# Kernel tuning notes

Hardware: AMD Instinct MI355X
Metric: run time of the kernel (lower is better)

The kernel has to match this reference:

```python
import jax, jax.numpy as jnp
import numpy as np

B, T, S, H = 8, 512, 512, 128


def setup_inputs() -> dict:
    key = jax.random.key(0)
    ks = jax.random.split(key, 8)
    query = jax.random.normal(ks[0], (B, T, H), dtype=jnp.float32)
    encoder_outputs = jax.random.normal(ks[1], (B, S, H), dtype=jnp.float32)
    src_lengths = jax.random.randint(ks[2], (B,), 1, S + 1)
    src_lengths = src_lengths.at[0].set(S)  # torch mask width == lengths.max() must equal S
    scale = 1.0 / np.sqrt(H)
    W_h = jax.random.normal(ks[3], (H, H), dtype=jnp.float32) * scale
    W_s = jax.random.normal(ks[4], (H, H), dtype=jnp.float32) * scale
    v = jax.random.normal(ks[5], (H,), dtype=jnp.float32) * scale
    W_out_w = jax.random.normal(ks[6], (H, 2 * H), dtype=jnp.float32) * (1.0 / np.sqrt(2 * H))
    W_out_b = jax.random.normal(ks[7], (H,), dtype=jnp.float32) * 0.01
    return {"query": query, "encoder_outputs": encoder_outputs,
            "src_lengths": src_lengths, "W_h": W_h, "W_s": W_s, "v": v,
            "W_out_w": W_out_w, "W_out_b": W_out_b}


def reference(query, encoder_outputs, src_lengths, W_h, W_s, v, W_out_w, W_out_b):
    # query: (B,T,H); encoder_outputs: (B,S,H)
    S_ = encoder_outputs.shape[1]
    WS = jnp.einsum('bth,oh->bto', query, W_s)            # (B,T,H)
    WH = jnp.einsum('bsh,oh->bso', encoder_outputs, W_h)  # (B,S,H)
    # additive scores: v^T tanh(W_s s_t + W_h h_i)  -> (B,T,S)
    scores = jnp.einsum('btsh,h->bts', jnp.tanh(WS[:, :, None, :] + WH[:, None, :, :]), v)
    mask = jnp.arange(S_) < src_lengths[:, None]          # (B,S)
    # faithful quirk: original zeroes (not -inf) masked scores before softmax
    scores = jnp.where(mask[:, None, :], scores, 0.0)
    attn = jax.nn.softmax(scores, axis=-1)                # (B,T,S)
    ct = jnp.einsum('bts,bsh->bth', attn, encoder_outputs)
    concat = jnp.concatenate([ct, query], axis=-1)        # (B,T,2H)
    return jnp.tanh(jnp.einsum('btc,oc->bto', concat, W_out_w) + W_out_b)
```

## Files before the change

kernel.cpp:

```cpp
#include <hip/hip_runtime.h>

#define NB 8
#define NT 512
#define NS 512
#define NH 128
#define C2LOG2E 2.8853900817779268f

__device__ __forceinline__ float fast_exp2(float x) { return __builtin_amdgcn_exp2f(x); }
__device__ __forceinline__ float fast_rcp(float x)  { return __builtin_amdgcn_rcpf(x); }
__device__ __forceinline__ float fast_tanh(float x) {
  float e = fast_exp2(x * C2LOG2E);
  return 1.0f - 2.0f * fast_rcp(e + 1.0f);
}

__device__ __forceinline__ float dot4(float4 a, float4 b) {
  return (a.x * b.x + a.y * b.y) + (a.z * b.z + a.w * b.w);
}

__device__ __forceinline__ float2 pair_acc2(float e0, float e1, float v0, float v1,
                                            float2 f0, float2 f1, float2 acc) {
  float2 P0, P1, num, den;
  P0.x = fmaf(e0, f0.x, 1.0f); P0.y = fmaf(e0, f0.y, 1.0f);
  P1.x = fmaf(e1, f1.x, 1.0f); P1.y = fmaf(e1, f1.y, 1.0f);
  num.x = fmaf(v0, P1.x, v1 * P0.x); num.y = fmaf(v0, P1.y, v1 * P0.y);
  den.x = P0.x * P1.x; den.y = P0.y * P1.y;
  acc.x = fmaf(num.x, fast_rcp(den.x), acc.x);
  acc.y = fmaf(num.y, fast_rcp(den.y), acc.y);
  return acc;
}

__device__ __forceinline__ float4 pair_acc(float e0, float e1, float v0, float v1,
                                           float4 f0, float4 f1, float4 acc) {
  float4 P0, P1, num, den;
  P0.x = fmaf(e0, f0.x, 1.0f); P0.y = fmaf(e0, f0.y, 1.0f);
  P0.z = fmaf(e0, f0.z, 1.0f); P0.w = fmaf(e0, f0.w, 1.0f);
  P1.x = fmaf(e1, f1.x, 1.0f); P1.y = fmaf(e1, f1.y, 1.0f);
  P1.z = fmaf(e1, f1.z, 1.0f); P1.w = fmaf(e1, f1.w, 1.0f);
  num.x = fmaf(v0, P1.x, v1 * P0.x); num.y = fmaf(v0, P1.y, v1 * P0.y);
  num.z = fmaf(v0, P1.z, v1 * P0.z); num.w = fmaf(v0, P1.w, v1 * P0.w);
  den.x = P0.x * P1.x; den.y = P0.y * P1.y;
  den.z = P0.z * P1.z; den.w = P0.w * P1.w;
  acc.x = fmaf(num.x, fast_rcp(den.x), acc.x);
  acc.y = fmaf(num.y, fast_rcp(den.y), acc.y);
  acc.z = fmaf(num.z, fast_rcp(den.z), acc.z);
  acc.w = fmaf(num.w, fast_rcp(den.w), acc.w);
  return acc;
}

__global__ __launch_bounds__(256) void bah_proj_kernel(
    const float* __restrict__ query, const float* __restrict__ enc,
    const float* __restrict__ W_s, const float* __restrict__ W_h,
    float* __restrict__ EWS, float* __restrict__ EWHT) {
  __shared__ __align__(16) float lds_w[64 * 132];
  __shared__ __align__(16) float lds_x[32 * 132];
  int blk = blockIdx.x;
  const bool is_wh = blk >= 256;
  const float* in = is_wh ? enc : query;
  const float* W  = is_wh ? W_h : W_s;
  blk &= 255;
  const int rb = blk >> 1, ch = blk & 1;
  const int r0 = rb * 32, c0 = ch * 64;
  const int tid = threadIdx.x;
  for (int i = tid; i < 2048; i += 256) {
    int r = i >> 5, c4 = i & 31;
    *(float4*)(lds_w + r * 132 + c4 * 4) =
        *(const float4*)(W + (c0 + r) * 128 + c4 * 4);
  }
  for (int i = tid; i < 1024; i += 256) {
    int r = i >> 5, c4 = i & 31;
    *(float4*)(lds_x + r * 132 + c4 * 4) =
        *(const float4*)(in + (r0 + r) * NH + c4 * 4);
  }
  __syncthreads();
  const int cg = tid & 31;
  const int rg = tid >> 5;
  float acc[4][2] = {{0,0},{0,0},{0,0},{0,0}};
  for (int k4 = 0; k4 < 32; ++k4) {
    float4 xa[4], wb[2];
    #pragma unroll
    for (int i = 0; i < 4; ++i)
      xa[i] = *(const float4*)(lds_x + (rg * 4 + i) * 132 + k4 * 4);
    #pragma unroll
    for (int m = 0; m < 2; ++m)
      wb[m] = *(const float4*)(lds_w + (cg + 32 * m) * 132 + k4 * 4);
    #pragma unroll
    for (int i = 0; i < 4; ++i)
      #pragma unroll
      for (int m = 0; m < 2; ++m)
        acc[i][m] += dot4(xa[i], wb[m]);
  }
  if (!is_wh) {
    #pragma unroll
    for (int i = 0; i < 4; ++i)
      #pragma unroll
      for (int m = 0; m < 2; ++m)
        EWS[(r0 + rg * 4 + i) * NH + c0 + cg + 32 * m] =
            fast_exp2(C2LOG2E * acc[i][m]);
  } else {
    __syncthreads();
    #pragma unroll
    for (int i = 0; i < 4; ++i)
      #pragma unroll
      for (int m = 0; m < 2; ++m)
        lds_x[(cg + 32 * m) * 33 + rg * 4 + i] = fast_exp2(C2LOG2E * acc[i][m]);
    __syncthreads();
    const int b = r0 >> 9, sl0 = r0 & 511;
    const int s_lane = tid & 31, hr = tid >> 5;
    #pragma unroll
    for (int j = 0; j < 8; ++j)
      EWHT[b * NH * NS + (c0 + hr * 8 + j) * NS + sl0 + s_lane] =
          lds_x[(hr * 8 + j) * 33 + s_lane];
  }
}

__global__ __launch_bounds__(256) void bah_score_kernel(
    const float* __restrict__ EWS, const float* __restrict__ EWHT,
    const float* __restrict__ v, const int* __restrict__ src_len,
    float* __restrict__ SC) {
  __shared__ __align__(16) float lds_et[8 * 132];
  __shared__ __align__(16) float lds_v[128];
  const int blk = blockIdx.x;
  const int sh = blk & 1, tt8 = (blk >> 1) & 63, bb = blk >> 7;
  const int s0 = sh * 256, t0 = tt8 * 8;
  const int len = src_len[bb];
  const int tid = threadIdx.x;
  const int tg = tid >> 7, sp = tid & 127;
  const int sbase = s0 + sp * 2;
  float* scb = SC + (bb * NT + t0) * NS;
  if (len <= s0) {
    float2 z = {0.f, 0.f};
    #pragma unroll
    for (int tt = 0; tt < 4; ++tt)
      *(float2*)(scb + (tg * 4 + tt) * NS + sbase) = z;
    return;
  }
  if (tid < 32) *(float4*)(lds_v + tid * 4) = *(const float4*)(v + tid * 4);
  { int r = tid >> 5, c4 = tid & 31;
    *(float4*)(lds_et + r * 132 + c4 * 4) =
        *(const float4*)(EWS + (bb * NT + t0 + r) * NH + c4 * 4); }
  __syncthreads();
  float V0 = 0.f;
  #pragma unroll
  for (int i = 0; i < 32; ++i) {
    float4 t4 = *(const float4*)(lds_v + i * 4);
    V0 += (t4.x + t4.y) + (t4.z + t4.w);
  }
  const float* et = lds_et + tg * 4 * 132;
  const float* fb = EWHT + bb * NH * NS + sbase;
  float2 acc2[4] = {{0,0},{0,0},{0,0},{0,0}};
  for (int ho = 0; ho < 16; ++ho) {
    const float* fh = fb + ho * 8 * NS;
    float2 F0 = *(const float2*)(fh + 0 * NS);
    float2 F1 = *(const float2*)(fh + 1 * NS);
    float2 F2 = *(const float2*)(fh + 2 * NS);
    float2 F3 = *(const float2*)(fh + 3 * NS);
    float2 F4 = *(const float2*)(fh + 4 * NS);
    float2 F5 = *(const float2*)(fh + 5 * NS);
    float2 F6 = *(const float2*)(fh + 6 * NS);
    float2 F7 = *(const float2*)(fh + 7 * NS);
    float4 va = *(const float4*)(lds_v + ho * 8);
    float4 vb = *(const float4*)(lds_v + ho * 8 + 4);
    #pragma unroll
    for (int tt = 0; tt < 4; ++tt) {
      float4 e0 = *(const float4*)(et + tt * 132 + ho * 8);
      float4 e1 = *(const float4*)(et + tt * 132 + ho * 8 + 4);
      acc2[tt] = pair_acc2(e0.x, e0.y, va.x, va.y, F0, F1, acc2[tt]);
      acc2[tt] = pair_acc2(e0.z, e0.w, va.z, va.w, F2, F3, acc2[tt]);
      acc2[tt] = pair_acc2(e1.x, e1.y, vb.x, vb.y, F4, F5, acc2[tt]);
      acc2[tt] = pair_acc2(e1.z, e1.w, vb.z, vb.w, F6, F7, acc2[tt]);
    }
  }
  #pragma unroll
  for (int tt = 0; tt < 4; ++tt) {
    float2 r;
    r.x = (sbase + 0 < len) ? fmaf(-2.f, acc2[tt].x, V0) : 0.f;
    r.y = (sbase + 1 < len) ? fmaf(-2.f, acc2[tt].y, V0) : 0.f;
    *(float2*)(scb + (tg * 4 + tt) * NS + sbase) = r;
  }
}

__global__ __launch_bounds__(256) void bah_ctx_kernel(
    const float* __restrict__ SC, const float* __restrict__ enc,
    float* __restrict__ CT) {
  __shared__ __align__(16) float lds_sc[4 * 516];
  __shared__ __align__(16) float lds_aT[512 * 4];
  __shared__ float red[16];
  const int tid = threadIdx.x;
  const int bb = blockIdx.x >> 7;
  const int t0 = (blockIdx.x & 127) * 4;
  for (int i = tid; i < 512; i += 256) {
    int r = i >> 7, c4 = i & 127;
    *(float4*)(lds_sc + r * 516 + c4 * 4) =
        *(const float4*)(SC + (bb * NT + t0 + r) * NS + c4 * 4);
  }
  __syncthreads();

  const int t = tid & 3;
  const int c = tid >> 2;
  const int wv = tid >> 6;
  float pv[8];
  float mx = -3.4e38f;
  #pragma unroll
  for (int k = 0; k < 8; ++k) {
    pv[k] = lds_sc[t * 516 + c + 64 * k];
    mx = fmaxf(mx, pv[k]);
  }
  #pragma unroll
  for (int msk = 4; msk <= 32; msk <<= 1)
    mx = fmaxf(mx, __shfl_xor(mx, msk, 64));
  if ((tid & 63) < 4) red[wv * 4 + t] = mx;
  __syncthreads();
  mx = fmaxf(fmaxf(red[t], red[4 + t]), fmaxf(red[8 + t], red[12 + t]));
  __syncthreads();
  float sum = 0.f;
  #pragma unroll
  for (int k = 0; k < 8; ++k) {
    pv[k] = fast_exp2((pv[k] - mx) * 1.4426950408889634f);
    sum += pv[k];
  }
  #pragma unroll
  for (int msk = 4; msk <= 32; msk <<= 1)
    sum += __shfl_xor(sum, msk, 64);
  if ((tid & 63) < 4) red[wv * 4 + t] = sum;
  __syncthreads();
  sum = (red[t] + red[4 + t]) + (red[8 + t] + red[12 + t]);
  const float rd = fast_rcp(sum);
  #pragma unroll
  for (int k = 0; k < 8; ++k)
    lds_aT[(c + 64 * k) * 4 + t] = pv[k] * rd;
  __syncthreads();

  const int hg = tid & 31, sg = tid >> 5;
  float4 a4[4] = {{0,0,0,0},{0,0,0,0},{0,0,0,0},{0,0,0,0}};
  const float* eb = enc + bb * NS * NH + hg * 4;
  for (int k = 0; k < 64; ++k) {
    int s = sg * 64 + k;
    float4 e = *(const float4*)(eb + s * NH);
    float4 w = *(const float4*)(lds_aT + s * 4);
    a4[0].x += w.x*e.x; a4[0].y += w.x*e.y; a4[0].z += w.x*e.z; a4[0].w += w.x*e.w;
    a4[1].x += w.y*e.x; a4[1].y += w.y*e.y; a4[1].z += w.y*e.z; a4[1].w += w.y*e.w;
    a4[2].x += w.z*e.x; a4[2].y += w.z*e.y; a4[2].z += w.z*e.z; a4[2].w += w.z*e.w;
    a4[3].x += w.w*e.x; a4[3].y += w.w*e.y; a4[3].z += w.w*e.z; a4[3].w += w.w*e.w;
  }
  #pragma unroll
  for (int i = 0; i < 4; ++i) {
    a4[i].x += __shfl_xor(a4[i].x, 32, 64);
    a4[i].y += __shfl_xor(a4[i].y, 32, 64);
    a4[i].z += __shfl_xor(a4[i].z, 32, 64);
    a4[i].w += __shfl_xor(a4[i].w, 32, 64);
  }
  float* lred = lds_sc;
  const int lane = tid & 63;
  if (lane < 32) {
    #pragma unroll
    for (int i = 0; i < 4; ++i)
      *(float4*)(lred + wv * 512 + i * 128 + hg * 4) = a4[i];
  }
  __syncthreads();
  if (tid < 128) {
    int tt = tid >> 5, hh = tid & 31;
    float4 s0 = *(const float4*)(lred + 0 * 512 + tt * 128 + hh * 4);
    float4 s1 = *(const float4*)(lred + 1 * 512 + tt * 128 + hh * 4);
    float4 s2 = *(const float4*)(lred + 2 * 512 + tt * 128 + hh * 4);
    float4 s3 = *(const float4*)(lred + 3 * 512 + tt * 128 + hh * 4);
    float4 o;
    o.x = (s0.x + s1.x) + (s2.x + s3.x);
    o.y = (s0.y + s1.y) + (s2.y + s3.y);
    o.z = (s0.z + s1.z) + (s2.z + s3.z);
    o.w = (s0.w + s1.w) + (s2.w + s3.w);
    *(float4*)(CT + (bb * NT + t0 + tt) * NH + hh * 4) = o;
  }
}

__global__ __launch_bounds__(256, 4) void bah_attn_fused(
    const float* __restrict__ EWS, const float* __restrict__ EWHT,
    const float* __restrict__ v, const float* __restrict__ enc,
    const int* __restrict__ src_len, float* __restrict__ CT) {
  __shared__ __align__(16) float lds_et[8 * 132];
  __shared__ __align__(16) float lds_v[128];
  __shared__ __align__(16) float lds_sc[8 * 516];
  __shared__ __align__(16) float lds_aT[512 * 8];
  __shared__ float red[32];
  const int tid = threadIdx.x;
  const int bb = blockIdx.x >> 6;
  const int t0 = (blockIdx.x & 63) * 8;
  const int len = src_len[bb];
  if (tid < 32) *(float4*)(lds_v + tid * 4) = *(const float4*)(v + tid * 4);
  { int r = tid >> 5, c4 = tid & 31;
    *(float4*)(lds_et + r * 132 + c4 * 4) =
        *(const float4*)(EWS + (bb * NT + t0 + r) * NH + c4 * 4); }
  __syncthreads();
  float V0 = 0.f;
  #pragma unroll
  for (int i = 0; i < 32; ++i) {
    float4 t4 = *(const float4*)(lds_v + i * 4);
    V0 += (t4.x + t4.y) + (t4.z + t4.w);
  }
  const int tg = tid >> 7, sp = tid & 127;
  const float* et = lds_et + tg * 4 * 132;
  const float* fb = EWHT + bb * NH * NS + sp * 4;
  float4 acc4[4] = {{0,0,0,0},{0,0,0,0},{0,0,0,0},{0,0,0,0}};
  for (int ho = 0; ho < 16; ++ho) {
    const float* fh = fb + ho * 8 * NS;
    float4 F0 = *(const float4*)(fh + 0 * NS);
    float4 F1 = *(const float4*)(fh + 1 * NS);
    float4 F2 = *(const float4*)(fh + 2 * NS);
    float4 F3 = *(const float4*)(fh + 3 * NS);
    float4 F4 = *(const float4*)(fh + 4 * NS);
    float4 F5 = *(const float4*)(fh + 5 * NS);
    float4 F6 = *(const float4*)(fh + 6 * NS);
    float4 F7 = *(const float4*)(fh + 7 * NS);
    float4 va = *(const float4*)(lds_v + ho * 8);
    float4 vb = *(const float4*)(lds_v + ho * 8 + 4);
    #pragma unroll
    for (int tt = 0; tt < 4; ++tt) {
      float4 e0 = *(const float4*)(et + tt * 132 + ho * 8);
      float4 e1 = *(const float4*)(et + tt * 132 + ho * 8 + 4);
      acc4[tt] = pair_acc(e0.x, e0.y, va.x, va.y, F0, F1, acc4[tt]);
      acc4[tt] = pair_acc(e0.z, e0.w, va.z, va.w, F2, F3, acc4[tt]);
      acc4[tt] = pair_acc(e1.x, e1.y, vb.x, vb.y, F4, F5, acc4[tt]);
      acc4[tt] = pair_acc(e1.z, e1.w, vb.z, vb.w, F6, F7, acc4[tt]);
    }
  }
  const int sbase = sp * 4;
  #pragma unroll
  for (int tt = 0; tt < 4; ++tt) {
    float4 r;
    r.x = (sbase + 0 < len) ? fmaf(-2.f, acc4[tt].x, V0) : 0.f;
    r.y = (sbase + 1 < len) ? fmaf(-2.f, acc4[tt].y, V0) : 0.f;
    r.z = (sbase + 2 < len) ? fmaf(-2.f, acc4[tt].z, V0) : 0.f;
    r.w = (sbase + 3 < len) ? fmaf(-2.f, acc4[tt].w, V0) : 0.f;
    *(float4*)(lds_sc + (tg * 4 + tt) * 516 + sbase) = r;
  }
  __syncthreads();
  const int t = tid & 7;
  const int c = tid >> 3;
  const int wid = tid >> 6;
  float pv[16];
  float mx = -3.4e38f;
  #pragma unroll
  for (int k = 0; k < 16; ++k) {
    pv[k] = lds_sc[t * 516 + c + 32 * k];
    mx = fmaxf(mx, pv[k]);
  }
  #pragma unroll
  for (int msk = 8; msk <= 32; msk <<= 1)
    mx = fmaxf(mx, __shfl_xor(mx, msk, 64));
  if ((tid & 63) < 8) red[wid * 8 + t] = mx;
  __syncthreads();
  mx = fmaxf(fmaxf(red[t], red[8 + t]), fmaxf(red[16 + t], red[24 + t]));
  __syncthreads();
  float sum = 0.f;
  #pragma unroll
  for (int k = 0; k < 16; ++k) {
    pv[k] = fast_exp2((pv[k] - mx) * 1.4426950408889634f);
    sum += pv[k];
  }
  #pragma unroll
  for (int msk = 8; msk <= 32; msk <<= 1)
    sum += __shfl_xor(sum, msk, 64);
  if ((tid & 63) < 8) red[wid * 8 + t] = sum;
  __syncthreads();
  sum = (red[t] + red[8 + t]) + (red[16 + t] + red[24 + t]);
  const float rd = fast_rcp(sum);
  #pragma unroll
  for (int k = 0; k < 16; ++k)
    lds_aT[(c + 32 * k) * 8 + t] = pv[k] * rd;
  __syncthreads();
  const int hg = tid & 31, sg = tid >> 5;
  float4 a8[8] = {{0,0,0,0},{0,0,0,0},{0,0,0,0},{0,0,0,0},
                  {0,0,0,0},{0,0,0,0},{0,0,0,0},{0,0,0,0}};
  const float* eb = enc + bb * NS * NH + hg * 4;
  for (int k = 0; k < 64; ++k) {
    int s = sg * 64 + k;
    float4 e  = *(const float4*)(eb + s * NH);
    float4 w0 = *(const float4*)(lds_aT + s * 8);
    float4 w1 = *(const float4*)(lds_aT + s * 8 + 4);
    a8[0].x += w0.x*e.x; a8[0].y += w0.x*e.y; a8[0].z += w0.x*e.z; a8[0].w += w0.x*e.w;
    a8[1].x += w0.y*e.x; a8[1].y += w0.y*e.y; a8[1].z += w0.y*e.z; a8[1].w += w0.y*e.w;
    a8[2].x += w0.z*e.x; a8[2].y += w0.z*e.y; a8[2].z += w0.z*e.z; a8[2].w += w0.z*e.w;
    a8[3].x += w0.w*e.x; a8[3].y += w0.w*e.y; a8[3].z += w0.w*e.z; a8[3].w += w0.w*e.w;
    a8[4].x += w1.x*e.x; a8[4].y += w1.x*e.y; a8[4].z += w1.x*e.z; a8[4].w += w1.x*e.w;
    a8[5].x += w1.y*e.x; a8[5].y += w1.y*e.y; a8[5].z += w1.y*e.z; a8[5].w += w1.y*e.w;
    a8[6].x += w1.z*e.x; a8[6].y += w1.z*e.y; a8[6].z += w1.z*e.z; a8[6].w += w1.z*e.w;
    a8[7].x += w1.w*e.x; a8[7].y += w1.w*e.y; a8[7].z += w1.w*e.z; a8[7].w += w1.w*e.w;
  }
  #pragma unroll
  for (int i = 0; i < 8; ++i) {
    a8[i].x += __shfl_xor(a8[i].x, 32, 64);
    a8[i].y += __shfl_xor(a8[i].y, 32, 64);
    a8[i].z += __shfl_xor(a8[i].z, 32, 64);
    a8[i].w += __shfl_xor(a8[i].w, 32, 64);
  }
  float* lred = lds_sc;
  const int wv = tid >> 6, lane = tid & 63;
  if (lane < 32) {
    #pragma unroll
    for (int i = 0; i < 8; ++i)
      *(float4*)(lred + wv * 1024 + i * 128 + lane * 4) = a8[i];
  }
  __syncthreads();
  { int tt2 = tid >> 5, hh = tid & 31;
    float4 s0 = *(const float4*)(lred + 0 * 1024 + tt2 * 128 + hh * 4);
    float4 s1 = *(const float4*)(lred + 1 * 1024 + tt2 * 128 + hh * 4);
    float4 s2 = *(const float4*)(lred + 2 * 1024 + tt2 * 128 + hh * 4);
    float4 s3 = *(const float4*)(lred + 3 * 1024 + tt2 * 128 + hh * 4);
    float4 o;
    o.x = (s0.x + s1.x) + (s2.x + s3.x);
    o.y = (s0.y + s1.y) + (s2.y + s3.y);
    o.z = (s0.z + s1.z) + (s2.z + s3.z);
    o.w = (s0.w + s1.w) + (s2.w + s3.w);
    *(float4*)(CT + (bb * NT + t0 + tt2) * NH + hh * 4) = o;
  }
}

__global__ __launch_bounds__(256) void bah_out_kernel(
    const float* __restrict__ CT, const float* __restrict__ query,
    const float* __restrict__ Wout, const float* __restrict__ bias,
    float* __restrict__ out) {
  __shared__ __align__(16) float lds_w[64 * 132];
  __shared__ __align__(16) float lds_x[16 * 260];
  const int rt = blockIdx.x >> 1, ch = blockIdx.x & 1;
  const int r0 = rt * 16, c0 = ch * 64;
  const int tid = threadIdx.x;
  for (int i = tid; i < 1024; i += 256) {
    int r = i >> 6, cc = (i & 63) * 4;
    float4 val = (cc < 128)
        ? *(const float4*)(CT + (r0 + r) * NH + cc)
        : *(const float4*)(query + (r0 + r) * NH + cc - 128);
    *(float4*)(lds_x + r * 260 + cc) = val;
  }
  const int cg = tid & 31;
  const int rg = tid >> 5;
  float acc[2][2] = {{0,0},{0,0}};
  for (int p = 0; p < 2; ++p) {
    __syncthreads();
    for (int i = tid; i < 2048; i += 256) {
      int r = i >> 5, c4 = i & 31;
      *(float4*)(lds_w + r * 132 + c4 * 4) =
          *(const float4*)(Wout + (c0 + r) * 256 + p * 128 + c4 * 4);
    }
    __syncthreads();
    for (int k4 = 0; k4 < 32; ++k4) {
      float4 xa[2], wb[2];
      #pragma unroll
      for (int i = 0; i < 2; ++i)
        xa[i] = *(const float4*)(lds_x + (rg * 2 + i) * 260 + p * 128 + k4 * 4);
      #pragma unroll
      for (int m = 0; m < 2; ++m)
        wb[m] = *(const float4*)(lds_w + (cg + 32 * m) * 132 + k4 * 4);
      #pragma unroll
      for (int i = 0; i < 2; ++i)
        #pragma unroll
        for (int m = 0; m < 2; ++m)
          acc[i][m] += dot4(xa[i], wb[m]);
    }
  }
  #pragma unroll
  for (int i = 0; i < 2; ++i)
    #pragma unroll
    for (int m = 0; m < 2; ++m)
      out[(r0 + rg * 2 + i) * NH + c0 + cg + 32 * m] =
          fast_tanh(acc[i][m] + bias[c0 + cg + 32 * m]);
}

extern "C" void kernel_launch(void* const* d_in, const int* in_sizes, int n_in,
                              void* d_out, int out_size, void* d_ws, size_t ws_size,
                              hipStream_t stream) {
  const float* query = (const float*)d_in[0];
  const float* enc   = (const float*)d_in[1];
  const int*   slen  = (const int*)d_in[2];
  const float* W_h   = (const float*)d_in[3];
  const float* W_s   = (const float*)d_in[4];
  const float* v     = (const float*)d_in[5];
  const float* Woutw = (const float*)d_in[6];
  const float* Woutb = (const float*)d_in[7];
  float* out = (float*)d_out;

  float* ws = (float*)d_ws;
  float* EWS  = ws;
  float* EWHT = ws + 524288;
  float* CT   = ws + 1048576;
  float* SC   = ws + 1572864;
  const bool have_sc = ws_size >= (size_t)(1572864 + 2097152) * sizeof(float);

  bah_proj_kernel<<<512, 256, 0, stream>>>(query, enc, W_s, W_h, EWS, EWHT);
  if (have_sc) {
    bah_score_kernel<<<1024, 256, 0, stream>>>(EWS, EWHT, v, slen, SC);
    bah_ctx_kernel<<<1024, 256, 0, stream>>>(SC, enc, CT);
  } else {
    bah_attn_fused<<<512, 256, 0, stream>>>(EWS, EWHT, v, enc, slen, CT);
  }
  bah_out_kernel<<<512, 256, 0, stream>>>(CT, query, Woutw, Woutb, out);
}
```

Measured before the change: 135.1 us.

## Fuse output projection into context kernel and split score work across H halves

The separate output-projection kernel is removed from the main path and its linear-plus-tanh is folded into the context kernel, reading a transposed W_out that the projection kernel now also produces in extra blocks. The score kernel now has each half of the block cover all 8 query rows over half of H, then combines the two partial sums through shared memory, instead of splitting rows. This saves one launch and a round-trip of the context tensor through global memory. In exchange it adds per-block GEMV work with global W reads in the ctx kernel, plus an extra barrier and LDS exchange in the score kernel.

```diff
diff --git a/kernel.cpp b/kernel.cpp
--- a/kernel.cpp
+++ b/kernel.cpp
@@ -50,10 +50,18 @@
 __global__ __launch_bounds__(256) void bah_proj_kernel(
     const float* __restrict__ query, const float* __restrict__ enc,
     const float* __restrict__ W_s, const float* __restrict__ W_h,
-    float* __restrict__ EWS, float* __restrict__ EWHT) {
+    const float* __restrict__ Wout,
+    float* __restrict__ EWS, float* __restrict__ EWHT, float* __restrict__ WTP) {
   __shared__ __align__(16) float lds_w[64 * 132];
   __shared__ __align__(16) float lds_x[32 * 132];
   int blk = blockIdx.x;
+  if (blk >= 512) {
+    int g = (blk - 512) * 256 + threadIdx.x;
+    int c = g >> 6, k4 = g & 63;
+    float4 w = *(const float4*)(Wout + c * 256 + k4 * 4);
+    *(float4*)(WTP + k4 * 512 + c * 4) = w;
+    return;
+  }
   const bool is_wh = blk >= 256;
   const float* in = is_wh ? enc : query;
   const float* W  = is_wh ? W_h : W_s;
@@ -119,6 +127,7 @@
     float* __restrict__ SC) {
   __shared__ __align__(16) float lds_et[8 * 132];
   __shared__ __align__(16) float lds_v[128];
+  __shared__ __align__(16) float lds_par[128 * 18];
   const int blk = blockIdx.x;
   const int sh = blk & 1, tt8 = (blk >> 1) & 63, bb = blk >> 7;
   const int s0 = sh * 256, t0 = tt8 * 8;
@@ -128,10 +137,12 @@
   const int sbase = s0 + sp * 2;
   float* scb = SC + (bb * NT + t0) * NS;
   if (len <= s0) {
-    float2 z = {0.f, 0.f};
-    #pragma unroll
-    for (int tt = 0; tt < 4; ++tt)
-      *(float2*)(scb + (tg * 4 + tt) * NS + sbase) = z;
+    if (tg == 0) {
+      float2 z = {0.f, 0.f};
+      #pragma unroll
+      for (int tt = 0; tt < 8; ++tt)
+        *(float2*)(scb + tt * NS + sbase) = z;
+    }
     return;
   }
   if (tid < 32) *(float4*)(lds_v + tid * 4) = *(const float4*)(v + tid * 4);
@@ -139,16 +150,12 @@
     *(float4*)(lds_et + r * 132 + c4 * 4) =
         *(const float4*)(EWS + (bb * NT + t0 + r) * NH + c4 * 4); }
   __syncthreads();
-  float V0 = 0.f;
-  #pragma unroll
-  for (int i = 0; i < 32; ++i) {
-    float4 t4 = *(const float4*)(lds_v + i * 4);
-    V0 += (t4.x + t4.y) + (t4.z + t4.w);
-  }
-  const float* et = lds_et + tg * 4 * 132;
-  const float* fb = EWHT + bb * NH * NS + sbase;
-  float2 acc2[4] = {{0,0},{0,0},{0,0},{0,0}};
-  for (int ho = 0; ho < 16; ++ho) {
+  const int h0 = tg * 64;
+  const float* fb = EWHT + bb * NH * NS + h0 * NS + sbase;
+  float2 acc2[8];
+  #pragma unroll
+  for (int i = 0; i < 8; ++i) { acc2[i].x = 0.f; acc2[i].y = 0.f; }
+  for (int ho = 0; ho < 8; ++ho) {
     const float* fh = fb + ho * 8 * NS;
     float2 F0 = *(const float2*)(fh + 0 * NS);
     float2 F1 = *(const float2*)(fh + 1 * NS);
@@ -158,30 +165,48 @@
     float2 F5 = *(const float2*)(fh + 5 * NS);
     float2 F6 = *(const float2*)(fh + 6 * NS);
     float2 F7 = *(const float2*)(fh + 7 * NS);
-    float4 va = *(const float4*)(lds_v + ho * 8);
-    float4 vb = *(const float4*)(lds_v + ho * 8 + 4);
-    #pragma unroll
-    for (int tt = 0; tt < 4; ++tt) {
-      float4 e0 = *(const float4*)(et + tt * 132 + ho * 8);
-      float4 e1 = *(const float4*)(et + tt * 132 + ho * 8 + 4);
+    float4 va = *(const float4*)(lds_v + h0 + ho * 8);
+    float4 vb = *(const float4*)(lds_v + h0 + ho * 8 + 4);
+    #pragma unroll
+    for (int tt = 0; tt < 8; ++tt) {
+      float4 e0 = *(const float4*)(lds_et + tt * 132 + h0 + ho * 8);
+      float4 e1 = *(const float4*)(lds_et + tt * 132 + h0 + ho * 8 + 4);
       acc2[tt] = pair_acc2(e0.x, e0.y, va.x, va.y, F0, F1, acc2[tt]);
       acc2[tt] = pair_acc2(e0.z, e0.w, va.z, va.w, F2, F3, acc2[tt]);
       acc2[tt] = pair_acc2(e1.x, e1.y, vb.x, vb.y, F4, F5, acc2[tt]);
       acc2[tt] = pair_acc2(e1.z, e1.w, vb.z, vb.w, F6, F7, acc2[tt]);
     }
   }
-  #pragma unroll
-  for (int tt = 0; tt < 4; ++tt) {
-    float2 r;
-    r.x = (sbase + 0 < len) ? fmaf(-2.f, acc2[tt].x, V0) : 0.f;
-    r.y = (sbase + 1 < len) ? fmaf(-2.f, acc2[tt].y, V0) : 0.f;
-    *(float2*)(scb + (tg * 4 + tt) * NS + sbase) = r;
-  }
-}
-
-__global__ __launch_bounds__(256) void bah_ctx_kernel(
+  if (tg == 1) {
+    #pragma unroll
+    for (int tt = 0; tt < 8; ++tt)
+      *(float2*)(lds_par + sp * 18 + tt * 2) = acc2[tt];
+  }
+  __syncthreads();
+  if (tg == 0) {
+    float V0 = 0.f;
+    #pragma unroll
+    for (int i = 0; i < 32; ++i) {
+      float4 t4 = *(const float4*)(lds_v + i * 4);
+      V0 += (t4.x + t4.y) + (t4.z + t4.w);
+    }
+    #pragma unroll
+    for (int tt = 0; tt < 8; ++tt) {
+      float2 oth = *(const float2*)(lds_par + sp * 18 + tt * 2);
+      float sx = acc2[tt].x + oth.x;
+      float sy = acc2[tt].y + oth.y;
+      float2 r;
+      r.x = (sbase + 0 < len) ? fmaf(-2.f, sx, V0) : 0.f;
+      r.y = (sbase + 1 < len) ? fmaf(-2.f, sy, V0) : 0.f;
+      *(float2*)(scb + tt * NS + sbase) = r;
+    }
+  }
+}
+
+__global__ __launch_bounds__(256) void bah_ctx_out_kernel(
     const float* __restrict__ SC, const float* __restrict__ enc,
-    float* __restrict__ CT) {
+    const float* __restrict__ query, const float* __restrict__ WTP,
+    const float* __restrict__ bias, float* __restrict__ out) {
   __shared__ __align__(16) float lds_sc[4 * 516];
   __shared__ __align__(16) float lds_aT[512 * 4];
   __shared__ float red[16];
@@ -268,8 +293,32 @@
     o.y = (s0.y + s1.y) + (s2.y + s3.y);
     o.z = (s0.z + s1.z) + (s2.z + s3.z);
     o.w = (s0.w + s1.w) + (s2.w + s3.w);
-    *(float4*)(CT + (bb * NT + t0 + tt) * NH + hh * 4) = o;
-  }
+    *(float4*)(lds_aT + tt * 128 + hh * 4) = o;
+    *(float4*)(lds_aT + 512 + tt * 128 + hh * 4) =
+        *(const float4*)(query + (bb * NT + t0 + tt) * NH + hh * 4);
+  }
+  __syncthreads();
+
+  const int cc = tid & 127, th = tid >> 7;
+  const float* x0 = lds_aT + (th * 2) * 128;
+  const float* x1 = x0 + 128;
+  const float* y0 = lds_aT + 512 + (th * 2) * 128;
+  const float* y1 = y0 + 128;
+  float a0 = 0.f, a1 = 0.f;
+  for (int k4 = 0; k4 < 32; ++k4) {
+    float4 w = *(const float4*)(WTP + k4 * 512 + cc * 4);
+    a0 += dot4(*(const float4*)(x0 + k4 * 4), w);
+    a1 += dot4(*(const float4*)(x1 + k4 * 4), w);
+  }
+  for (int k4 = 32; k4 < 64; ++k4) {
+    float4 w = *(const float4*)(WTP + k4 * 512 + cc * 4);
+    a0 += dot4(*(const float4*)(y0 + (k4 - 32) * 4), w);
+    a1 += dot4(*(const float4*)(y1 + (k4 - 32) * 4), w);
+  }
+  const float bc = bias[cc];
+  float* ob = out + (bb * NT + t0 + th * 2) * NH;
+  ob[cc]      = fast_tanh(a0 + bc);
+  ob[NH + cc] = fast_tanh(a1 + bc);
 }
 
 __global__ __launch_bounds__(256, 4) void bah_attn_fused(
@@ -482,14 +531,18 @@
   float* EWHT = ws + 524288;
   float* CT   = ws + 1048576;
   float* SC   = ws + 1572864;
-  const bool have_sc = ws_size >= (size_t)(1572864 + 2097152) * sizeof(float);
-
-  bah_proj_kernel<<<512, 256, 0, stream>>>(query, enc, W_s, W_h, EWS, EWHT);
+  float* WTP  = ws + 3670016;
+  const bool have_sc =
+      ws_size >= (size_t)(3670016 + 32768) * sizeof(float);
+
+  bah_proj_kernel<<<544, 256, 0, stream>>>(query, enc, W_s, W_h, Woutw,
+                                           EWS, EWHT, WTP);
   if (have_sc) {
     bah_score_kernel<<<1024, 256, 0, stream>>>(EWS, EWHT, v, slen, SC);
-    bah_ctx_kernel<<<1024, 256, 0, stream>>>(SC, enc, CT);
+    bah_ctx_out_kernel<<<1024, 256, 0, stream>>>(SC, enc, query, WTP,
+                                                 Woutb, out);
   } else {
     bah_attn_fused<<<512, 256, 0, stream>>>(EWS, EWHT, v, enc, slen, CT);
-  }
-  bah_out_kernel<<<512, 256, 0, stream>>>(CT, query, Woutw, Woutb, out);
-}
+    bah_out_kernel<<<512, 256, 0, stream>>>(CT, query, Woutw, Woutb, out);
+  }
+}
```

Result: faster. 128.2 us (-5.1%).
